# Kernel tuning notes

Hardware: AMD Instinct MI355X
Metric: run time of the kernel (lower is better)

The kernel has to match this reference:

```python
import jax, jax.numpy as jnp
import numpy as np

B, S, H, NH = 2, 2048, 1024, 16
PH = H // NH  # per-head size = 64


def setup_inputs() -> dict:
    key = jax.random.key(0)
    ks = jax.random.split(key, 12)
    scale = 0.02
    inp = {
        "key": jax.random.normal(ks[0], (B, S, H), jnp.float32),
        "value": jax.random.normal(ks[1], (B, S, H), jnp.float32),
        "query": jax.random.normal(ks[2], (B, S, H), jnp.float32),
        "mask": jax.random.uniform(ks[3], (B, 1, S, S), jnp.float32),
        "i": 0,
        "Wq": jax.random.normal(ks[4], (H, H), jnp.float32) * scale,
        "bq": jnp.zeros((H,), jnp.float32),
        "Wk": jax.random.normal(ks[5], (H, H), jnp.float32) * scale,
        "bk": jnp.zeros((H,), jnp.float32),
        "Wv": jax.random.normal(ks[6], (H, H), jnp.float32) * scale,
        "bv": jnp.zeros((H,), jnp.float32),
        "Wo": jax.random.normal(ks[7], (H, H), jnp.float32) * scale,
        "bo": jnp.zeros((H,), jnp.float32),
    }
    return inp


def reference(key, value, query, mask, i, Wq, bq, Wk, bk, Wv, bv, Wo, bo):
    # Linear projections (torch nn.Linear: x @ W.T + b), then split heads -> [B, NH, S, PH]
    def proj(x, W, b):
        return (x @ W.T + b).reshape(B, S, NH, PH).transpose(0, 2, 1, 3)

    q = proj(query, Wq, bq)
    k = proj(key, Wk, bk)
    v = proj(value, Wv, bv)

    # scores: [B, NH, S, S]; scale then MULTIPLICATIVE mask (as in the original)
    scores = jnp.einsum('bhqd,bhkd->bhqk', q, k) / jnp.sqrt(jnp.float32(PH))
    scores = scores * mask
    probs = jax.nn.softmax(scores, axis=-1)  # dropout p=0 -> identity

    # context: [B, NH, S, PH] -> merge heads -> [B, S, H]
    ctx = jnp.einsum('bhqk,bhkd->bhqd', probs, v)
    ctx = ctx.transpose(0, 2, 1, 3).reshape(B, S, H)
    return ctx @ Wo.T + bo
```

## Files before the change

kernel.cpp:

```cpp
#include <hip/hip_runtime.h>

typedef unsigned short ushort_t;
typedef __attribute__((ext_vector_type(8))) __bf16 bf16x8;
typedef __attribute__((ext_vector_type(4))) __bf16 bf16x4;
typedef __attribute__((ext_vector_type(4))) float f32x4;

__device__ inline float bf2f(ushort_t u) {
  union { unsigned int i; float f; } v; v.i = ((unsigned int)u) << 16; return v.f;
}
__device__ inline ushort_t f2bf(float f) {
  union { float f; unsigned int i; } v; v.f = f;
  unsigned int r = (v.i + 0x7fffu + ((v.i >> 16) & 1u)) >> 16;
  return (ushort_t)r;
}

__global__ void detect_dtype_kernel(const ushort_t* __restrict__ w,
                                    int* __restrict__ flag) {
  int lane = threadIdx.x & 63;
  int cnt = 0;
  for (int i = 0; i < 4; i++) {
    float a = fabsf(bf2f(w[lane * 4 + i]));
    if (a >= 1e-4f && a <= 0.5f) cnt++;
  }
  for (int off = 1; off < 64; off <<= 1) cnt += __shfl_xor(cnt, off, 64);
  if (threadIdx.x == 0) *flag = (cnt >= 192) ? 1 : 0;
}

__device__ inline float ld1(const void* src, size_t idx, int isbf) {
  return isbf ? bf2f(((const ushort_t*)src)[idx]) : ((const float*)src)[idx];
}

struct pre8 { float4 a, b; };
__device__ inline pre8 pref8(const void* src, size_t idx, int isbf) {
  pre8 u;
  if (isbf) {
    u.a = *(const float4*)((const ushort_t*)src + idx);
    u.b = u.a;
  } else {
    const float* s = (const float*)src + idx;
    u.a = *(const float4*)s;
    u.b = *(const float4*)(s + 4);
  }
  return u;
}
__device__ inline void commit8(ushort_t* dst, pre8 u, int isbf) {
  if (isbf) {
    *(float4*)dst = u.a;
  } else {
    union { bf16x8 v; ushort_t u8[8]; } t;
    t.u8[0] = f2bf(u.a.x); t.u8[1] = f2bf(u.a.y); t.u8[2] = f2bf(u.a.z); t.u8[3] = f2bf(u.a.w);
    t.u8[4] = f2bf(u.b.x); t.u8[5] = f2bf(u.b.y); t.u8[6] = f2bf(u.b.z); t.u8[7] = f2bf(u.b.w);
    *(bf16x8*)dst = t.v;
  }
}
__device__ inline void cvt8(ushort_t* dst, const void* src, size_t idx, int isbf) {
  commit8(dst, pref8(src, idx, isbf), isbf);
}

#define NW_ ((size_t)1024 * 1024)
#define NX_ ((size_t)4096 * 1024)
#define NM_ ((size_t)2 * 2048 * 2048)

__global__ __launch_bounds__(256) void cvt_all_kernel(
    const void* xq, const void* xk, const void* xv,
    const void* wq, const void* wk, const void* wv, const void* wo,
    ushort_t* __restrict__ dst, const int* __restrict__ flag) {
  int seg = blockIdx.z;
  const void* src; size_t n, doff;
  switch (seg) {
    case 0: src = wq; n = NW_; doff = 0;                 break;
    case 1: src = wk; n = NW_; doff = NW_;               break;
    case 2: src = wv; n = NW_; doff = 2 * NW_;           break;
    case 3: src = wo; n = NW_; doff = 3 * NW_;           break;
    case 4: src = xq; n = NX_; doff = 4 * NW_;           break;
    case 5: src = xk; n = NX_; doff = 4 * NW_ + NX_;     break;
    default: src = xv; n = NX_; doff = 4 * NW_ + 2 * NX_; break;
  }
  size_t i = ((size_t)blockIdx.x * 256 + threadIdx.x) * 8;
  if (i >= n) return;
  cvt8(&dst[doff + i], src, i, *flag);
}

__global__ __launch_bounds__(256) void transpose_mask_kernel(
    const void* __restrict__ M, ushort_t* __restrict__ Mt,
    const int* __restrict__ flag) {
  __shared__ ushort_t T[64][72];
  const int f = *flag;
  const int tid = threadIdx.x;
  const int r = tid >> 2, c = (tid & 3) * 16;
  const int b = blockIdx.z;
  const int q0 = blockIdx.x * 64, k0 = blockIdx.y * 64;
  const size_t src = (size_t)b * 2048 * 2048 + (size_t)(q0 + r) * 2048 + k0 + c;
  cvt8(&T[r][c],     M, src, f);
  cvt8(&T[r][c + 8], M, src + 8, f);
  __syncthreads();
  union { bf16x8 v; ushort_t u[8]; } o0, o1;
  for (int i = 0; i < 8; i++) o0.u[i] = T[c + i][r];
  for (int i = 0; i < 8; i++) o1.u[i] = T[c + 8 + i][r];
  ushort_t* dst = Mt + (size_t)b * 2048 * 2048;
  *(bf16x8*)&dst[(size_t)(k0 + r) * 2048 + q0 + c]     = o0.v;
  *(bf16x8*)&dst[(size_t)(k0 + r) * 2048 + q0 + c + 8] = o1.v;
}

#define KDIM 1024
#define NDIM 1024

__device__ __forceinline__ void gld_lds16(ushort_t* lds, const ushort_t* g) {
  __builtin_amdgcn_global_load_lds(
      (const __attribute__((address_space(1))) void*)g,
      (__attribute__((address_space(3))) void*)lds, 16, 0, 0);
}

template <int MODE>
__global__ __launch_bounds__(256) void gemm_fast_kernel(
    const ushort_t* __restrict__ X0, const ushort_t* __restrict__ X1,
    const ushort_t* __restrict__ X2,
    const ushort_t* __restrict__ W0, const ushort_t* __restrict__ W1,
    const ushort_t* __restrict__ W2,
    const void* __restrict__ B0, const void* __restrict__ B1,
    const void* __restrict__ B2,
    void* __restrict__ O0, void* __restrict__ O1, void* __restrict__ O2,
    const int* __restrict__ flag) {
  __shared__ ushort_t As[128 * 64];
  __shared__ ushort_t Bs[128 * 64];
  const int z = blockIdx.z;
  const ushort_t* X = z == 0 ? X0 : z == 1 ? X1 : X2;
  const ushort_t* W = z == 0 ? W0 : z == 1 ? W1 : W2;
  const void* Bias  = z == 0 ? B0 : z == 1 ? B1 : B2;
  void* Out         = z == 0 ? O0 : z == 1 ? O1 : O2;
  const int f = *flag;

  const int tid = threadIdx.x;
  const int wave = tid >> 6, lane = tid & 63;
  const int g = lane >> 4, l16 = lane & 15;
  const int m0 = blockIdx.y * 128, n0 = blockIdx.x * 128;
  const int wm = (wave >> 1) * 64, wn = (wave & 1) * 64;
  const int lr = lane >> 3;
  const int lc = (lane & 7) ^ lr;

  f32x4 acc[4][4] = {};

  for (int k0 = 0; k0 < KDIM; k0 += 64) {
#pragma unroll
    for (int q = 0; q < 4; q++) {
      const int row = wave * 32 + q * 8;
      gld_lds16(&As[row * 64], &X[(size_t)(m0 + row + lr) * KDIM + k0 + lc * 8]);
      gld_lds16(&Bs[row * 64], &W[(size_t)(n0 + row + lr) * KDIM + k0 + lc * 8]);
    }
    __syncthreads();

    bf16x8 af[2][4], bfr[2][4];
#pragma unroll
    for (int kk = 0; kk < 2; kk++)
#pragma unroll
      for (int i = 0; i < 4; i++) {
        const int cs = ((g + 4 * kk) ^ (l16 & 7)) * 8;
        af[kk][i]  = *(const bf16x8*)&As[(wm + i * 16 + l16) * 64 + cs];
        bfr[kk][i] = *(const bf16x8*)&Bs[(wn + i * 16 + l16) * 64 + cs];
      }
#pragma unroll
    for (int kk = 0; kk < 2; kk++)
#pragma unroll
      for (int i = 0; i < 4; i++)
#pragma unroll
        for (int j = 0; j < 4; j++)
          acc[i][j] = __builtin_amdgcn_mfma_f32_16x16x32_bf16(
              af[kk][i], bfr[kk][j], acc[i][j], 0, 0, 0);
    __syncthreads();
  }

  for (int i = 0; i < 4; i++)
    for (int j = 0; j < 4; j++)
      for (int r = 0; r < 4; r++) {
        int m = m0 + wm + i * 16 + g * 4 + r;
        int n = n0 + wn + j * 16 + l16;
        float v = acc[i][j][r] + ld1(Bias, n, f);
        if (MODE == 0) {
          if (f) ((ushort_t*)Out)[(size_t)m * NDIM + n] = f2bf(v);
          else   ((float*)Out)[(size_t)m * NDIM + n] = v;
        } else {
          int b = m >> 11, s = m & 2047, h = n >> 6, d = n & 63;
          ((ushort_t*)Out)[((((size_t)b * 16 + h) * 2048) + s) * 64 + d] = f2bf(v);
        }
      }
}

#define BK 32

template <int MODE>
__device__ inline void gemm_body(const void* __restrict__ X,
                                 const void* __restrict__ W,
                                 const void* __restrict__ Bias,
                                 void* __restrict__ Out,
                                 int xbf, int wbf, int bbf, int obf) {
  __shared__ ushort_t As[128][BK + 8];
  __shared__ ushort_t Bs[128][BK + 8];
  const int tid = threadIdx.x;
  const int wave = tid >> 6, lane = tid & 63;
  const int g = lane >> 4, l16 = lane & 15;
  const int m0 = blockIdx.y * 128, n0 = blockIdx.x * 128;
  const int wm = (wave >> 1) * 64, wn = (wave & 1) * 64;

  f32x4 acc[4][4] = {};
  const int r0 = tid >> 2, c0 = (tid & 3) * 8;
  const size_t ia0 = (size_t)(m0 + r0) * KDIM + c0;
  const size_t ia1 = (size_t)(m0 + r0 + 64) * KDIM + c0;
  const size_t ib0 = (size_t)(n0 + r0) * KDIM + c0;
  const size_t ib1 = (size_t)(n0 + r0 + 64) * KDIM + c0;

  pre8 pa0 = pref8(X, ia0, xbf), pa1 = pref8(X, ia1, xbf);
  pre8 pb0 = pref8(W, ib0, wbf), pb1 = pref8(W, ib1, wbf);

  for (int k0 = 0; k0 < KDIM; k0 += BK) {
    commit8(&As[r0][c0],      pa0, xbf);
    commit8(&As[r0 + 64][c0], pa1, xbf);
    commit8(&Bs[r0][c0],      pb0, wbf);
    commit8(&Bs[r0 + 64][c0], pb1, wbf);
    const int kn = (k0 + BK) & (KDIM - 1);
    pa0 = pref8(X, ia0 + kn, xbf); pa1 = pref8(X, ia1 + kn, xbf);
    pb0 = pref8(W, ib0 + kn, wbf); pb1 = pref8(W, ib1 + kn, wbf);
    __syncthreads();
    bf16x8 af[4], bfr[4];
    for (int i = 0; i < 4; i++) af[i]  = *(const bf16x8*)&As[wm + i * 16 + l16][g * 8];
    for (int j = 0; j < 4; j++) bfr[j] = *(const bf16x8*)&Bs[wn + j * 16 + l16][g * 8];
    for (int i = 0; i < 4; i++)
      for (int j = 0; j < 4; j++)
        acc[i][j] = __builtin_amdgcn_mfma_f32_16x16x32_bf16(af[i], bfr[j], acc[i][j], 0, 0, 0);
    __syncthreads();
  }
  for (int i = 0; i < 4; i++)
    for (int j = 0; j < 4; j++)
      for (int r = 0; r < 4; r++) {
        int m = m0 + wm + i * 16 + g * 4 + r;
        int n = n0 + wn + j * 16 + l16;
        float v = acc[i][j][r] + ld1(Bias, n, bbf);
        if (MODE == 0) {
          if (obf) ((ushort_t*)Out)[(size_t)m * NDIM + n] = f2bf(v);
          else     ((float*)Out)[(size_t)m * NDIM + n] = v;
        } else {
          int b = m >> 11, s = m & 2047, h = n >> 6, d = n & 63;
          ((ushort_t*)Out)[((((size_t)b * 16 + h) * 2048) + s) * 64 + d] = f2bf(v);
        }
      }
}

__global__ __launch_bounds__(256) void proj_qkv_fb_kernel(
    const void* __restrict__ query, const void* __restrict__ key,
    const void* __restrict__ value,
    const void* __restrict__ Wq, const void* __restrict__ bq,
    const void* __restrict__ Wk, const void* __restrict__ bk,
    const void* __restrict__ Wv, const void* __restrict__ bv,
    ushort_t* __restrict__ Q, ushort_t* __restrict__ K, ushort_t* __restrict__ V,
    const int* __restrict__ flag) {
  int f = *flag;
  int z = blockIdx.z;
  const void* X = z == 0 ? query : z == 1 ? key : value;
  const void* W = z == 0 ? Wq : z == 1 ? Wk : Wv;
  const void* B = z == 0 ? bq : z == 1 ? bk : bv;
  ushort_t* O  = z == 0 ? Q  : z == 1 ? K  : V;
  gemm_body<1>(X, W, B, O, f, f, f, 1);
}

__global__ __launch_bounds__(256) void out_proj_fb_kernel(
    const ushort_t* __restrict__ X, const void* __restrict__ W,
    const void* __restrict__ B, void* __restrict__ O,
    const int* __restrict__ flag) {
  int f = *flag;
  gemm_body<0>(X, W, B, O, 1, f, f, f);
}

__global__ __launch_bounds__(256) void transpose_v_kernel(
    const ushort_t* __restrict__ Vin, ushort_t* __restrict__ Vout) {
  __shared__ ushort_t T[64][72];
  const int tid = threadIdx.x;
  const int r = tid >> 2, c = (tid & 3) * 16;
  const int bh = blockIdx.y;
  const int s0 = blockIdx.x * 64;
  const ushort_t* src = Vin + (size_t)bh * 2048 * 64;
  *(bf16x8*)&T[r][c]     = *(const bf16x8*)&src[(size_t)(s0 + r) * 64 + c];
  *(bf16x8*)&T[r][c + 8] = *(const bf16x8*)&src[(size_t)(s0 + r) * 64 + c + 8];
  __syncthreads();
  union { bf16x8 v; ushort_t u[8]; } o0, o1;
  for (int i = 0; i < 8; i++) o0.u[i] = T[c + i][r];
  for (int i = 0; i < 8; i++) o1.u[i] = T[c + 8 + i][r];
  ushort_t* dst = Vout + (size_t)bh * 64 * 2048;
  *(bf16x8*)&dst[(size_t)r * 2048 + s0 + c]     = o0.v;
  *(bf16x8*)&dst[(size_t)r * 2048 + s0 + c + 8] = o1.v;
}

__global__ __launch_bounds__(256, 2) void flash_attn128_kernel(
    const ushort_t* __restrict__ Q, const ushort_t* __restrict__ K,
    const ushort_t* __restrict__ Vt, const ushort_t* __restrict__ Mt,
    ushort_t* __restrict__ ctx) {
  __shared__ ushort_t Ks[64 * 72];
  __shared__ ushort_t Vs[64 * 72];
  __shared__ ushort_t MQ[8448];
  __shared__ ushort_t Ps[4][32 * 72];

  const int tid = threadIdx.x;
  const int wave = tid >> 6, lane = tid & 63;
  const int g = lane >> 4, l16 = lane & 15;
  const int bh = blockIdx.x;
  const int b = bh >> 4, h = bh & 15;
  const int q0 = blockIdx.y * 128;

  const ushort_t* Qh = Q + (size_t)bh * 2048 * 64;
  const ushort_t* Kh = K + (size_t)bh * 2048 * 64;
  const ushort_t* Vh = Vt + (size_t)bh * 64 * 2048;
  const ushort_t* Mh = Mt + (size_t)b * 2048 * 2048 + q0;

  {
    const int qr = tid >> 1, qc = (tid & 1) * 32;
#pragma unroll
    for (int ch = 0; ch < 4; ch++) {
      union { bf16x8 v; ushort_t u[8]; } a;
      a.v = *(const bf16x8*)&Qh[(size_t)(q0 + qr) * 64 + qc + ch * 8];
      for (int i = 0; i < 8; i++) a.u[i] = f2bf(bf2f(a.u[i]) * 0.125f);
      *(bf16x8*)&MQ[qr * 66 + qc + ch * 8] = a.v;
    }
  }
  __syncthreads();
  bf16x8 aq[2][2];
#pragma unroll
  for (int t = 0; t < 2; t++)
#pragma unroll
    for (int kk = 0; kk < 2; kk++)
      aq[t][kk] = *(const bf16x8*)&MQ[(wave * 32 + t * 16 + l16) * 66 + kk * 32 + g * 8];

  float lpart[2][4] = {};
  f32x4 o_acc[2][4] = {};

  const int r = tid >> 2, c = (tid & 3) * 16;
  const int mc = (tid & 3) * 32;

  bf16x8 kr0 = *(const bf16x8*)&Kh[(size_t)r * 64 + c];
  bf16x8 kr1 = *(const bf16x8*)&Kh[(size_t)r * 64 + c + 8];
  bf16x8 vr0 = *(const bf16x8*)&Vh[(size_t)r * 2048 + c];
  bf16x8 vr1 = *(const bf16x8*)&Vh[(size_t)r * 2048 + c + 8];
  bf16x8 pm0 = *(const bf16x8*)&Mh[(size_t)r * 2048 + mc];
  bf16x8 pm1 = *(const bf16x8*)&Mh[(size_t)r * 2048 + mc + 8];
  bf16x8 pm2 = *(const bf16x8*)&Mh[(size_t)r * 2048 + mc + 16];
  bf16x8 pm3 = *(const bf16x8*)&Mh[(size_t)r * 2048 + mc + 24];

  for (int kt0 = 0; kt0 < 2048; kt0 += 64) {
    __syncthreads();
    *(bf16x8*)&Ks[r * 72 + c]      = kr0;
    *(bf16x8*)&Ks[r * 72 + c + 8]  = kr1;
    *(bf16x8*)&Vs[r * 72 + c]      = vr0;
    *(bf16x8*)&Vs[r * 72 + c + 8]  = vr1;
    *(bf16x8*)&MQ[r * 132 + mc]      = pm0;
    *(bf16x8*)&MQ[r * 132 + mc + 8]  = pm1;
    *(bf16x8*)&MQ[r * 132 + mc + 16] = pm2;
    *(bf16x8*)&MQ[r * 132 + mc + 24] = pm3;
    __syncthreads();

    const int ktn = (kt0 + 64) & 2047;
    kr0 = *(const bf16x8*)&Kh[(size_t)(ktn + r) * 64 + c];
    kr1 = *(const bf16x8*)&Kh[(size_t)(ktn + r) * 64 + c + 8];
    vr0 = *(const bf16x8*)&Vh[(size_t)r * 2048 + ktn + c];
    vr1 = *(const bf16x8*)&Vh[(size_t)r * 2048 + ktn + c + 8];
    pm0 = *(const bf16x8*)&Mh[(size_t)(ktn + r) * 2048 + mc];
    pm1 = *(const bf16x8*)&Mh[(size_t)(ktn + r) * 2048 + mc + 8];
    pm2 = *(const bf16x8*)&Mh[(size_t)(ktn + r) * 2048 + mc + 16];
    pm3 = *(const bf16x8*)&Mh[(size_t)(ktn + r) * 2048 + mc + 24];

    f32x4 sc[2][4] = {};
#pragma unroll
    for (int j = 0; j < 4; j++) {
      bf16x8 bk0 = *(const bf16x8*)&Ks[(j * 16 + l16) * 72 + g * 8];
      bf16x8 bk1 = *(const bf16x8*)&Ks[(j * 16 + l16) * 72 + 32 + g * 8];
#pragma unroll
      for (int t = 0; t < 2; t++) {
        sc[t][j] = __builtin_amdgcn_mfma_f32_16x16x32_bf16(aq[t][0], bk0, sc[t][j], 0, 0, 0);
        sc[t][j] = __builtin_amdgcn_mfma_f32_16x16x32_bf16(aq[t][1], bk1, sc[t][j], 0, 0, 0);
      }
    }

#pragma unroll
    for (int t = 0; t < 2; t++)
#pragma unroll
      for (int j = 0; j < 4; j++) {
        union { bf16x4 v; ushort_t u[4]; } m4;
        m4.v = *(const bf16x4*)&MQ[(j * 16 + l16) * 132 + wave * 32 + t * 16 + g * 4];
#pragma unroll
        for (int rr = 0; rr < 4; rr++) {
          float s = fminf(sc[t][j][rr] * bf2f(m4.u[rr]), 80.f);
          float p = __expf(s);
          unsigned int pb = __float_as_uint(p);
          lpart[t][rr] += __uint_as_float(pb & 0xffff0000u);
          Ps[wave][(t * 16 + g * 4 + rr) * 72 + j * 16 + l16] = (ushort_t)(pb >> 16);
        }
      }
    asm volatile("" ::: "memory");

    bf16x8 pf00 = *(const bf16x8*)&Ps[wave][(l16) * 72 + g * 8];
    bf16x8 pf01 = *(const bf16x8*)&Ps[wave][(l16) * 72 + 32 + g * 8];
    bf16x8 pf10 = *(const bf16x8*)&Ps[wave][(16 + l16) * 72 + g * 8];
    bf16x8 pf11 = *(const bf16x8*)&Ps[wave][(16 + l16) * 72 + 32 + g * 8];
#pragma unroll
    for (int jd = 0; jd < 4; jd++) {
      bf16x8 vf0 = *(const bf16x8*)&Vs[(jd * 16 + l16) * 72 + g * 8];
      bf16x8 vf1 = *(const bf16x8*)&Vs[(jd * 16 + l16) * 72 + 32 + g * 8];
      o_acc[0][jd] = __builtin_amdgcn_mfma_f32_16x16x32_bf16(pf00, vf0, o_acc[0][jd], 0, 0, 0);
      o_acc[0][jd] = __builtin_amdgcn_mfma_f32_16x16x32_bf16(pf01, vf1, o_acc[0][jd], 0, 0, 0);
      o_acc[1][jd] = __builtin_amdgcn_mfma_f32_16x16x32_bf16(pf10, vf0, o_acc[1][jd], 0, 0, 0);
      o_acc[1][jd] = __builtin_amdgcn_mfma_f32_16x16x32_bf16(pf11, vf1, o_acc[1][jd], 0, 0, 0);
    }
  }

#pragma unroll
  for (int t = 0; t < 2; t++) {
    float rl[4];
#pragma unroll
    for (int rr = 0; rr < 4; rr++) {
      float l = lpart[t][rr];
      l += __shfl_xor(l, 1, 64);
      l += __shfl_xor(l, 2, 64);
      l += __shfl_xor(l, 4, 64);
      l += __shfl_xor(l, 8, 64);
      rl[rr] = 1.0f / l;
    }
#pragma unroll
    for (int jd = 0; jd < 4; jd++)
#pragma unroll
      for (int rr = 0; rr < 4; rr++) {
        int qrow = q0 + wave * 32 + t * 16 + g * 4 + rr;
        ctx[((size_t)b * 2048 + qrow) * 1024 + h * 64 + jd * 16 + l16] =
            f2bf(o_acc[t][jd][rr] * rl[rr]);
      }
  }
}

#define FS 72

template <int PRET>
__global__ __launch_bounds__(256, 4) void flash_attn_kernel(
    const ushort_t* __restrict__ Q, const ushort_t* __restrict__ K,
    const ushort_t* __restrict__ V, const void* __restrict__ mask,
    ushort_t* __restrict__ ctx, const int* __restrict__ flag) {
  __shared__ ushort_t QsM[64][FS];
  __shared__ ushort_t Ks[64][FS];
  __shared__ ushort_t Vs[64][FS];
  __shared__ ushort_t Ps[4][16][FS];

  const int mbf = *flag;
  const int tid = threadIdx.x;
  const int wave = tid >> 6, lane = tid & 63;
  const int g = lane >> 4, l16 = lane & 15;
  const int bh = blockIdx.x;
  const int b = bh >> 4, h = bh & 15;
  const int q0 = blockIdx.y * 64;

  const ushort_t* Qh = Q + (size_t)bh * 2048 * 64;
  const ushort_t* Kh = K + (size_t)bh * 2048 * 64;
  const ushort_t* Vh = PRET ? V + (size_t)bh * 64 * 2048
                            : V + (size_t)bh * 2048 * 64;
  const int mrow = wave * 16 + g * 4;
  const int r = tid >> 2, c = (tid & 3) * 16;
  const size_t mstage = (size_t)b * 2048 * 2048 + (size_t)(q0 + r) * 2048 + c;

  {
    union { bf16x8 v; ushort_t u[8]; } a0, a1;
    a0.v = *(const bf16x8*)&Qh[(size_t)(q0 + r) * 64 + c];
    a1.v = *(const bf16x8*)&Qh[(size_t)(q0 + r) * 64 + c + 8];
    for (int i = 0; i < 8; i++) {
      a0.u[i] = f2bf(bf2f(a0.u[i]) * 0.125f);
      a1.u[i] = f2bf(bf2f(a1.u[i]) * 0.125f);
    }
    *(bf16x8*)&QsM[r][c]     = a0.v;
    *(bf16x8*)&QsM[r][c + 8] = a1.v;
  }
  __syncthreads();
  const bf16x8 aq0 = *(const bf16x8*)&QsM[wave * 16 + l16][g * 8];
  const bf16x8 aq1 = *(const bf16x8*)&QsM[wave * 16 + l16][32 + g * 8];

  float lpart[4] = {0.f, 0.f, 0.f, 0.f};
  f32x4 o_acc[4] = {};

  bf16x8 kr0 = *(const bf16x8*)&Kh[(size_t)r * 64 + c];
  bf16x8 kr1 = *(const bf16x8*)&Kh[(size_t)r * 64 + c + 8];
  bf16x8 vr0, vr1;
  if (PRET) {
    vr0 = *(const bf16x8*)&Vh[(size_t)r * 2048 + c];
    vr1 = *(const bf16x8*)&Vh[(size_t)r * 2048 + c + 8];
  } else {
    vr0 = *(const bf16x8*)&Vh[(size_t)r * 64 + c];
    vr1 = *(const bf16x8*)&Vh[(size_t)r * 64 + c + 8];
  }
  pre8 pm0 = pref8(mask, mstage, mbf);
  pre8 pm1 = pref8(mask, mstage + 8, mbf);

  for (int kt0 = 0; kt0 < 2048; kt0 += 64) {
    __syncthreads();
    *(bf16x8*)&Ks[r][c]     = kr0;
    *(bf16x8*)&Ks[r][c + 8] = kr1;
    if (PRET) {
      *(bf16x8*)&Vs[r][c]     = vr0;
      *(bf16x8*)&Vs[r][c + 8] = vr1;
    } else {
      union { bf16x8 v; ushort_t u[8]; } a0, a1;
      a0.v = vr0; a1.v = vr1;
      for (int i = 0; i < 8; i++) Vs[c + i][r] = a0.u[i];
      for (int i = 0; i < 8; i++) Vs[c + 8 + i][r] = a1.u[i];
    }
    commit8(&QsM[r][c],     pm0, mbf);
    commit8(&QsM[r][c + 8], pm1, mbf);
    __syncthreads();

    const int ktn = (kt0 + 64) & 2047;
    kr0 = *(const bf16x8*)&Kh[(size_t)(ktn + r) * 64 + c];
    kr1 = *(const bf16x8*)&Kh[(size_t)(ktn + r) * 64 + c + 8];
    if (PRET) {
      vr0 = *(const bf16x8*)&Vh[(size_t)r * 2048 + ktn + c];
      vr1 = *(const bf16x8*)&Vh[(size_t)r * 2048 + ktn + c + 8];
    } else {
      vr0 = *(const bf16x8*)&Vh[(size_t)(ktn + r) * 64 + c];
      vr1 = *(const bf16x8*)&Vh[(size_t)(ktn + r) * 64 + c + 8];
    }
    pm0 = pref8(mask, mstage + ktn, mbf);
    pm1 = pref8(mask, mstage + ktn + 8, mbf);

    f32x4 sc[4] = {};
#pragma unroll
    for (int j = 0; j < 4; j++) {
      bf16x8 bk0 = *(const bf16x8*)&Ks[j * 16 + l16][g * 8];
      bf16x8 bk1 = *(const bf16x8*)&Ks[j * 16 + l16][32 + g * 8];
      sc[j] = __builtin_amdgcn_mfma_f32_16x16x32_bf16(aq0, bk0, sc[j], 0, 0, 0);
      sc[j] = __builtin_amdgcn_mfma_f32_16x16x32_bf16(aq1, bk1, sc[j], 0, 0, 0);
    }

#pragma unroll
    for (int j = 0; j < 4; j++)
#pragma unroll
      for (int rr = 0; rr < 4; rr++) {
        float m = bf2f(QsM[mrow + rr][j * 16 + l16]);
        float s = fminf(sc[j][rr] * m, 80.f);
        float p = __expf(s);
        unsigned int pb = __float_as_uint(p);
        lpart[rr] += __uint_as_float(pb & 0xffff0000u);
        Ps[wave][g * 4 + rr][j * 16 + l16] = (ushort_t)(pb >> 16);
      }
    asm volatile("" ::: "memory");

    bf16x8 pf0 = *(const bf16x8*)&Ps[wave][l16][g * 8];
    bf16x8 pf1 = *(const bf16x8*)&Ps[wave][l16][32 + g * 8];
#pragma unroll
    for (int jd = 0; jd < 4; jd++) {
      bf16x8 vf0 = *(const bf16x8*)&Vs[jd * 16 + l16][g * 8];
      bf16x8 vf1 = *(const bf16x8*)&Vs[jd * 16 + l16][32 + g * 8];
      o_acc[jd] = __builtin_amdgcn_mfma_f32_16x16x32_bf16(pf0, vf0, o_acc[jd], 0, 0, 0);
      o_acc[jd] = __builtin_amdgcn_mfma_f32_16x16x32_bf16(pf1, vf1, o_acc[jd], 0, 0, 0);
    }
  }

  float rl[4];
  for (int rr = 0; rr < 4; rr++) {
    float l = lpart[rr];
    l += __shfl_xor(l, 1, 64);
    l += __shfl_xor(l, 2, 64);
    l += __shfl_xor(l, 4, 64);
    l += __shfl_xor(l, 8, 64);
    rl[rr] = 1.0f / l;
  }
  for (int jd = 0; jd < 4; jd++)
    for (int rr = 0; rr < 4; rr++) {
      int qrow = q0 + mrow + rr;
      ctx[((size_t)b * 2048 + qrow) * 1024 + h * 64 + jd * 16 + l16] =
          f2bf(o_acc[jd][rr] * rl[rr]);
    }
}

extern "C" void kernel_launch(void* const* d_in, const int* in_sizes, int n_in,
                              void* d_out, int out_size, void* d_ws, size_t ws_size,
                              hipStream_t stream) {
  (void)in_sizes; (void)n_in; (void)out_size;
  const void* key   = d_in[0];
  const void* value = d_in[1];
  const void* query = d_in[2];
  const void* mask  = d_in[3];
  const void* Wq = d_in[5];
  const void* bq = d_in[6];
  const void* Wk = d_in[7];
  const void* bk = d_in[8];
  const void* Wv = d_in[9];
  const void* bv = d_in[10];
  const void* Wo = d_in[11];
  const void* bo = d_in[12];

  const size_t E = (size_t)2 * 2048 * 1024;
  ushort_t* Qw  = (ushort_t*)d_ws;
  ushort_t* Kw  = Qw + E;
  ushort_t* Vw  = Kw + E;
  ushort_t* CTX = Vw + E;
  int* flag = (int*)(CTX + E);
  ushort_t* Vt   = (ushort_t*)((char*)flag + 256);
  ushort_t* conv = Vt + E;

  const size_t need_pret = 4 * E * 2 + 256 + E * 2;
  const size_t need_W   = need_pret + 4 * NW_ * 2;
  const size_t need_WX  = need_W + 3 * NX_ * 2;
  const size_t need_all = need_WX + NM_ * 2;
  const int pret  = ws_size >= need_pret ? 1 : 0;
  const int convW = (pret && ws_size >= need_W)   ? 1 : 0;
  const int convX = (pret && ws_size >= need_WX)  ? 1 : 0;
  const int convM = (pret && ws_size >= need_all) ? 1 : 0;

  detect_dtype_kernel<<<1, 64, 0, stream>>>((const ushort_t*)Wq, flag);

  if (convW) {
    int nseg = convX ? 7 : 4;
    int nx   = convX ? 2048 : 512;
    cvt_all_kernel<<<dim3(nx, 1, nseg), 256, 0, stream>>>(
        query, key, value, Wq, Wk, Wv, Wo, conv, flag);
  }
  const ushort_t* Wq_c = conv;
  const ushort_t* Wk_c = conv + NW_;
  const ushort_t* Wv_c = conv + 2 * NW_;
  const ushort_t* Wo_c = conv + 3 * NW_;
  const ushort_t* Xq_c = conv + 4 * NW_;
  const ushort_t* Xk_c = conv + 4 * NW_ + NX_;
  const ushort_t* Xv_c = conv + 4 * NW_ + 2 * NX_;
  ushort_t* Mt = conv + 4 * NW_ + 3 * NX_;

  if (convM) {
    transpose_mask_kernel<<<dim3(32, 32, 2), 256, 0, stream>>>(mask, Mt, flag);
  }

  if (convW && convX) {
    gemm_fast_kernel<1><<<dim3(8, 32, 3), 256, 0, stream>>>(
        Xq_c, Xk_c, Xv_c, Wq_c, Wk_c, Wv_c, bq, bk, bv,
        Qw, Kw, Vw, flag);
  } else {
    proj_qkv_fb_kernel<<<dim3(8, 32, 3), 256, 0, stream>>>(
        query, key, value, Wq, bq, Wk, bk, Wv, bv, Qw, Kw, Vw, flag);
  }

  if (pret) {
    transpose_v_kernel<<<dim3(32, 32), 256, 0, stream>>>(Vw, Vt);
    if (convM) {
      flash_attn128_kernel<<<dim3(32, 16), 256, 0, stream>>>(Qw, Kw, Vt, Mt, CTX);
    } else {
      flash_attn_kernel<1><<<dim3(32, 32), 256, 0, stream>>>(Qw, Kw, Vt, mask, CTX, flag);
    }
  } else {
    flash_attn_kernel<0><<<dim3(32, 32), 256, 0, stream>>>(Qw, Kw, Vw, mask, CTX, flag);
  }

  if (convW) {
    gemm_fast_kernel<0><<<dim3(8, 32, 1), 256, 0, stream>>>(
        CTX, CTX, CTX, Wo_c, Wo_c, Wo_c, bo, bo, bo,
        d_out, d_out, d_out, flag);
  } else {
    out_proj_fb_kernel<<<dim3(8, 32), 256, 0, stream>>>(CTX, Wo, bo, d_out, flag);
  }
}
```

Baseline: 330.1 us.

## Split attention over key halves, fuse mask transpose into prep, narrow out-proj tiles

Flash attention is split into two key-range halves via a grid z dimension, writing unnormalized fp32 partial outputs and row sums that a new combine kernel merges and normalizes into bf16 context. The mask transpose is folded into the input/weight conversion kernel as an extra segment, saving a launch. The output projection GEMM uses 64-wide N tiles to double block count. This raises parallelism for undersubscribed kernels at the cost of extra fp32 partial traffic, workspace, and an additional launch.

```diff
diff --git a/kernel.cpp b/kernel.cpp
--- a/kernel.cpp
+++ b/kernel.cpp
@@ -61,45 +61,45 @@
 #define NX_ ((size_t)4096 * 1024)
 #define NM_ ((size_t)2 * 2048 * 2048)
 
-__global__ __launch_bounds__(256) void cvt_all_kernel(
+__global__ __launch_bounds__(256) void prep_kernel(
     const void* xq, const void* xk, const void* xv,
     const void* wq, const void* wk, const void* wv, const void* wo,
-    ushort_t* __restrict__ dst, const int* __restrict__ flag) {
-  int seg = blockIdx.z;
-  const void* src; size_t n, doff;
-  switch (seg) {
-    case 0: src = wq; n = NW_; doff = 0;                 break;
-    case 1: src = wk; n = NW_; doff = NW_;               break;
-    case 2: src = wv; n = NW_; doff = 2 * NW_;           break;
-    case 3: src = wo; n = NW_; doff = 3 * NW_;           break;
-    case 4: src = xq; n = NX_; doff = 4 * NW_;           break;
-    case 5: src = xk; n = NX_; doff = 4 * NW_ + NX_;     break;
-    default: src = xv; n = NX_; doff = 4 * NW_ + 2 * NX_; break;
-  }
-  size_t i = ((size_t)blockIdx.x * 256 + threadIdx.x) * 8;
-  if (i >= n) return;
-  cvt8(&dst[doff + i], src, i, *flag);
-}
-
-__global__ __launch_bounds__(256) void transpose_mask_kernel(
-    const void* __restrict__ M, ushort_t* __restrict__ Mt,
+    const void* mask, ushort_t* __restrict__ dst, ushort_t* __restrict__ Mt,
     const int* __restrict__ flag) {
   __shared__ ushort_t T[64][72];
+  const int seg = blockIdx.z;
   const int f = *flag;
-  const int tid = threadIdx.x;
-  const int r = tid >> 2, c = (tid & 3) * 16;
-  const int b = blockIdx.z;
-  const int q0 = blockIdx.x * 64, k0 = blockIdx.y * 64;
-  const size_t src = (size_t)b * 2048 * 2048 + (size_t)(q0 + r) * 2048 + k0 + c;
-  cvt8(&T[r][c],     M, src, f);
-  cvt8(&T[r][c + 8], M, src + 8, f);
-  __syncthreads();
-  union { bf16x8 v; ushort_t u[8]; } o0, o1;
-  for (int i = 0; i < 8; i++) o0.u[i] = T[c + i][r];
-  for (int i = 0; i < 8; i++) o1.u[i] = T[c + 8 + i][r];
-  ushort_t* dst = Mt + (size_t)b * 2048 * 2048;
-  *(bf16x8*)&dst[(size_t)(k0 + r) * 2048 + q0 + c]     = o0.v;
-  *(bf16x8*)&dst[(size_t)(k0 + r) * 2048 + q0 + c + 8] = o1.v;
+  if (seg < 7) {
+    const void* src; size_t n, doff;
+    switch (seg) {
+      case 0: src = wq; n = NW_; doff = 0;                 break;
+      case 1: src = wk; n = NW_; doff = NW_;               break;
+      case 2: src = wv; n = NW_; doff = 2 * NW_;           break;
+      case 3: src = wo; n = NW_; doff = 3 * NW_;           break;
+      case 4: src = xq; n = NX_; doff = 4 * NW_;           break;
+      case 5: src = xk; n = NX_; doff = 4 * NW_ + NX_;     break;
+      default: src = xv; n = NX_; doff = 4 * NW_ + 2 * NX_; break;
+    }
+    size_t i = ((size_t)blockIdx.x * 256 + threadIdx.x) * 8;
+    if (i >= n) return;
+    cvt8(&dst[doff + i], src, i, f);
+  } else {
+    const int x = blockIdx.x;
+    const int b = x >> 10, rem = x & 1023;
+    const int q0 = (rem & 31) * 64, k0 = (rem >> 5) * 64;
+    const int tid = threadIdx.x;
+    const int r = tid >> 2, c = (tid & 3) * 16;
+    const size_t src = (size_t)b * 2048 * 2048 + (size_t)(q0 + r) * 2048 + k0 + c;
+    cvt8(&T[r][c],     mask, src, f);
+    cvt8(&T[r][c + 8], mask, src + 8, f);
+    __syncthreads();
+    union { bf16x8 v; ushort_t u[8]; } o0, o1;
+    for (int i = 0; i < 8; i++) o0.u[i] = T[c + i][r];
+    for (int i = 0; i < 8; i++) o1.u[i] = T[c + 8 + i][r];
+    ushort_t* d = Mt + (size_t)b * 2048 * 2048;
+    *(bf16x8*)&d[(size_t)(k0 + r) * 2048 + q0 + c]     = o0.v;
+    *(bf16x8*)&d[(size_t)(k0 + r) * 2048 + q0 + c + 8] = o1.v;
+  }
 }
 
 #define KDIM 1024
@@ -111,7 +111,7 @@
       (__attribute__((address_space(3))) void*)lds, 16, 0, 0);
 }
 
-template <int MODE>
+template <int MODE, int NT>
 __global__ __launch_bounds__(256) void gemm_fast_kernel(
     const ushort_t* __restrict__ X0, const ushort_t* __restrict__ X1,
     const ushort_t* __restrict__ X2,
@@ -121,8 +121,9 @@
     const void* __restrict__ B2,
     void* __restrict__ O0, void* __restrict__ O1, void* __restrict__ O2,
     const int* __restrict__ flag) {
+  constexpr int NJ = NT / 32;
   __shared__ ushort_t As[128 * 64];
-  __shared__ ushort_t Bs[128 * 64];
+  __shared__ ushort_t Bs[NT * 64];
   const int z = blockIdx.z;
   const ushort_t* X = z == 0 ? X0 : z == 1 ? X1 : X2;
   const ushort_t* W = z == 0 ? W0 : z == 1 ? W1 : W2;
@@ -133,44 +134,50 @@
   const int tid = threadIdx.x;
   const int wave = tid >> 6, lane = tid & 63;
   const int g = lane >> 4, l16 = lane & 15;
-  const int m0 = blockIdx.y * 128, n0 = blockIdx.x * 128;
-  const int wm = (wave >> 1) * 64, wn = (wave & 1) * 64;
+  const int m0 = blockIdx.y * 128, n0 = blockIdx.x * NT;
+  const int wm = (wave >> 1) * 64, wn = (wave & 1) * (NT / 2);
   const int lr = lane >> 3;
   const int lc = (lane & 7) ^ lr;
 
-  f32x4 acc[4][4] = {};
+  f32x4 acc[4][NJ] = {};
 
   for (int k0 = 0; k0 < KDIM; k0 += 64) {
 #pragma unroll
     for (int q = 0; q < 4; q++) {
       const int row = wave * 32 + q * 8;
       gld_lds16(&As[row * 64], &X[(size_t)(m0 + row + lr) * KDIM + k0 + lc * 8]);
+    }
+#pragma unroll
+    for (int q = 0; q < NT / 32; q++) {
+      const int row = wave * (NT / 4) + q * 8;
       gld_lds16(&Bs[row * 64], &W[(size_t)(n0 + row + lr) * KDIM + k0 + lc * 8]);
     }
     __syncthreads();
 
-    bf16x8 af[2][4], bfr[2][4];
+    bf16x8 af[2][4], bfr[2][NJ];
+#pragma unroll
+    for (int kk = 0; kk < 2; kk++) {
+      const int cs = ((g + 4 * kk) ^ (l16 & 7)) * 8;
+#pragma unroll
+      for (int i = 0; i < 4; i++)
+        af[kk][i]  = *(const bf16x8*)&As[(wm + i * 16 + l16) * 64 + cs];
+#pragma unroll
+      for (int j = 0; j < NJ; j++)
+        bfr[kk][j] = *(const bf16x8*)&Bs[(wn + j * 16 + l16) * 64 + cs];
+    }
 #pragma unroll
     for (int kk = 0; kk < 2; kk++)
 #pragma unroll
-      for (int i = 0; i < 4; i++) {
-        const int cs = ((g + 4 * kk) ^ (l16 & 7)) * 8;
-        af[kk][i]  = *(const bf16x8*)&As[(wm + i * 16 + l16) * 64 + cs];
-        bfr[kk][i] = *(const bf16x8*)&Bs[(wn + i * 16 + l16) * 64 + cs];
-      }
-#pragma unroll
-    for (int kk = 0; kk < 2; kk++)
-#pragma unroll
       for (int i = 0; i < 4; i++)
 #pragma unroll
-        for (int j = 0; j < 4; j++)
+        for (int j = 0; j < NJ; j++)
           acc[i][j] = __builtin_amdgcn_mfma_f32_16x16x32_bf16(
               af[kk][i], bfr[kk][j], acc[i][j], 0, 0, 0);
     __syncthreads();
   }
 
   for (int i = 0; i < 4; i++)
-    for (int j = 0; j < 4; j++)
+    for (int j = 0; j < NJ; j++)
       for (int r = 0; r < 4; r++) {
         int m = m0 + wm + i * 16 + g * 4 + r;
         int n = n0 + wn + j * 16 + l16;
@@ -288,10 +295,12 @@
   *(bf16x8*)&dst[(size_t)r * 2048 + s0 + c + 8] = o1.v;
 }
 
+template <int SPLIT>
 __global__ __launch_bounds__(256, 2) void flash_attn128_kernel(
     const ushort_t* __restrict__ Q, const ushort_t* __restrict__ K,
     const ushort_t* __restrict__ Vt, const ushort_t* __restrict__ Mt,
-    ushort_t* __restrict__ ctx) {
+    ushort_t* __restrict__ ctx, float* __restrict__ Opart,
+    float* __restrict__ Lpart) {
   __shared__ ushort_t Ks[64 * 72];
   __shared__ ushort_t Vs[64 * 72];
   __shared__ ushort_t MQ[8448];
@@ -303,6 +312,8 @@
   const int bh = blockIdx.x;
   const int b = bh >> 4, h = bh & 15;
   const int q0 = blockIdx.y * 128;
+  const int z = SPLIT ? blockIdx.z : 0;
+  const int kbase = z * 1024, kend = SPLIT ? kbase + 1024 : 2048;
 
   const ushort_t* Qh = Q + (size_t)bh * 2048 * 64;
   const ushort_t* Kh = K + (size_t)bh * 2048 * 64;
@@ -333,16 +344,16 @@
   const int r = tid >> 2, c = (tid & 3) * 16;
   const int mc = (tid & 3) * 32;
 
-  bf16x8 kr0 = *(const bf16x8*)&Kh[(size_t)r * 64 + c];
-  bf16x8 kr1 = *(const bf16x8*)&Kh[(size_t)r * 64 + c + 8];
-  bf16x8 vr0 = *(const bf16x8*)&Vh[(size_t)r * 2048 + c];
-  bf16x8 vr1 = *(const bf16x8*)&Vh[(size_t)r * 2048 + c + 8];
-  bf16x8 pm0 = *(const bf16x8*)&Mh[(size_t)r * 2048 + mc];
-  bf16x8 pm1 = *(const bf16x8*)&Mh[(size_t)r * 2048 + mc + 8];
-  bf16x8 pm2 = *(const bf16x8*)&Mh[(size_t)r * 2048 + mc + 16];
-  bf16x8 pm3 = *(const bf16x8*)&Mh[(size_t)r * 2048 + mc + 24];
-
-  for (int kt0 = 0; kt0 < 2048; kt0 += 64) {
+  bf16x8 kr0 = *(const bf16x8*)&Kh[(size_t)(kbase + r) * 64 + c];
+  bf16x8 kr1 = *(const bf16x8*)&Kh[(size_t)(kbase + r) * 64 + c + 8];
+  bf16x8 vr0 = *(const bf16x8*)&Vh[(size_t)r * 2048 + kbase + c];
+  bf16x8 vr1 = *(const bf16x8*)&Vh[(size_t)r * 2048 + kbase + c + 8];
+  bf16x8 pm0 = *(const bf16x8*)&Mh[(size_t)(kbase + r) * 2048 + mc];
+  bf16x8 pm1 = *(const bf16x8*)&Mh[(size_t)(kbase + r) * 2048 + mc + 8];
+  bf16x8 pm2 = *(const bf16x8*)&Mh[(size_t)(kbase + r) * 2048 + mc + 16];
+  bf16x8 pm3 = *(const bf16x8*)&Mh[(size_t)(kbase + r) * 2048 + mc + 24];
+
+  for (int kt0 = kbase; kt0 < kend; kt0 += 64) {
     __syncthreads();
     *(bf16x8*)&Ks[r * 72 + c]      = kr0;
     *(bf16x8*)&Ks[r * 72 + c + 8]  = kr1;
@@ -408,27 +419,76 @@
     }
   }
 
-#pragma unroll
-  for (int t = 0; t < 2; t++) {
-    float rl[4];
-#pragma unroll
-    for (int rr = 0; rr < 4; rr++) {
-      float l = lpart[t][rr];
-      l += __shfl_xor(l, 1, 64);
-      l += __shfl_xor(l, 2, 64);
-      l += __shfl_xor(l, 4, 64);
-      l += __shfl_xor(l, 8, 64);
-      rl[rr] = 1.0f / l;
-    }
-#pragma unroll
-    for (int jd = 0; jd < 4; jd++)
+  if (SPLIT) {
+    float* Ow = Opart + (size_t)z * ((size_t)2 * 2048 * 1024);
+    float* Lw = Lpart + (size_t)z * (32 * 2048);
+#pragma unroll
+    for (int t = 0; t < 2; t++) {
+      float ls[4];
 #pragma unroll
       for (int rr = 0; rr < 4; rr++) {
-        int qrow = q0 + wave * 32 + t * 16 + g * 4 + rr;
-        ctx[((size_t)b * 2048 + qrow) * 1024 + h * 64 + jd * 16 + l16] =
-            f2bf(o_acc[t][jd][rr] * rl[rr]);
+        float l = lpart[t][rr];
+        l += __shfl_xor(l, 1, 64);
+        l += __shfl_xor(l, 2, 64);
+        l += __shfl_xor(l, 4, 64);
+        l += __shfl_xor(l, 8, 64);
+        ls[rr] = l;
       }
-  }
+      if (l16 == 0)
+#pragma unroll
+        for (int rr = 0; rr < 4; rr++)
+          Lw[(size_t)bh * 2048 + q0 + wave * 32 + t * 16 + g * 4 + rr] = ls[rr];
+#pragma unroll
+      for (int jd = 0; jd < 4; jd++)
+#pragma unroll
+        for (int rr = 0; rr < 4; rr++) {
+          int qrow = q0 + wave * 32 + t * 16 + g * 4 + rr;
+          Ow[((size_t)b * 2048 + qrow) * 1024 + h * 64 + jd * 16 + l16] =
+              o_acc[t][jd][rr];
+        }
+    }
+  } else {
+#pragma unroll
+    for (int t = 0; t < 2; t++) {
+      float rl[4];
+#pragma unroll
+      for (int rr = 0; rr < 4; rr++) {
+        float l = lpart[t][rr];
+        l += __shfl_xor(l, 1, 64);
+        l += __shfl_xor(l, 2, 64);
+        l += __shfl_xor(l, 4, 64);
+        l += __shfl_xor(l, 8, 64);
+        rl[rr] = 1.0f / l;
+      }
+#pragma unroll
+      for (int jd = 0; jd < 4; jd++)
+#pragma unroll
+        for (int rr = 0; rr < 4; rr++) {
+          int qrow = q0 + wave * 32 + t * 16 + g * 4 + rr;
+          ctx[((size_t)b * 2048 + qrow) * 1024 + h * 64 + jd * 16 + l16] =
+              f2bf(o_acc[t][jd][rr] * rl[rr]);
+        }
+    }
+  }
+}
+
+__global__ __launch_bounds__(256) void combine_kernel(
+    const float* __restrict__ O0, const float* __restrict__ O1,
+    const float* __restrict__ L0, const float* __restrict__ L1,
+    ushort_t* __restrict__ ctx) {
+  size_t i = ((size_t)blockIdx.x * 256 + threadIdx.x) * 4;
+  int h = (int)((i & 1023) >> 6);
+  size_t s = (i >> 10) & 2047, b = i >> 21;
+  size_t li = (b * 16 + h) * 2048 + s;
+  float rl = 1.0f / (L0[li] + L1[li]);
+  float4 a = *(const float4*)&O0[i];
+  float4 c = *(const float4*)&O1[i];
+  union { bf16x4 v; ushort_t u[4]; } o;
+  o.u[0] = f2bf((a.x + c.x) * rl);
+  o.u[1] = f2bf((a.y + c.y) * rl);
+  o.u[2] = f2bf((a.z + c.z) * rl);
+  o.u[3] = f2bf((a.w + c.w) * rl);
+  *(bf16x4*)&ctx[i] = o.v;
 }
 
 #define FS 72
@@ -595,23 +655,28 @@
   int* flag = (int*)(CTX + E);
   ushort_t* Vt   = (ushort_t*)((char*)flag + 256);
   ushort_t* conv = Vt + E;
-
-  const size_t need_pret = 4 * E * 2 + 256 + E * 2;
-  const size_t need_W   = need_pret + 4 * NW_ * 2;
-  const size_t need_WX  = need_W + 3 * NX_ * 2;
-  const size_t need_all = need_WX + NM_ * 2;
+  ushort_t* Mt = conv + 4 * NW_ + 3 * NX_;
+  float* Opart = (float*)(Mt + NM_);
+  float* Lpart = Opart + 2 * E;
+
+  const size_t need_pret  = 4 * E * 2 + 256 + E * 2;
+  const size_t need_W     = need_pret + 4 * NW_ * 2;
+  const size_t need_WX    = need_W + 3 * NX_ * 2;
+  const size_t need_all   = need_WX + NM_ * 2;
+  const size_t need_split = need_all + 2 * E * 4 + 2 * (size_t)32 * 2048 * 4;
   const int pret  = ws_size >= need_pret ? 1 : 0;
   const int convW = (pret && ws_size >= need_W)   ? 1 : 0;
   const int convX = (pret && ws_size >= need_WX)  ? 1 : 0;
   const int convM = (pret && ws_size >= need_all) ? 1 : 0;
+  const int ksplit = (convM && ws_size >= need_split) ? 1 : 0;
 
   detect_dtype_kernel<<<1, 64, 0, stream>>>((const ushort_t*)Wq, flag);
 
   if (convW) {
-    int nseg = convX ? 7 : 4;
-    int nx   = convX ? 2048 : 512;
-    cvt_all_kernel<<<dim3(nx, 1, nseg), 256, 0, stream>>>(
-        query, key, value, Wq, Wk, Wv, Wo, conv, flag);
+    int nseg = convM ? 8 : (convX ? 7 : 4);
+    int nx   = (convX || convM) ? 2048 : 512;
+    prep_kernel<<<dim3(nx, 1, nseg), 256, 0, stream>>>(
+        query, key, value, Wq, Wk, Wv, Wo, mask, conv, Mt, flag);
   }
   const ushort_t* Wq_c = conv;
   const ushort_t* Wk_c = conv + NW_;
@@ -620,14 +685,9 @@
   const ushort_t* Xq_c = conv + 4 * NW_;
   const ushort_t* Xk_c = conv + 4 * NW_ + NX_;
   const ushort_t* Xv_c = conv + 4 * NW_ + 2 * NX_;
-  ushort_t* Mt = conv + 4 * NW_ + 3 * NX_;
-
-  if (convM) {
-    transpose_mask_kernel<<<dim3(32, 32, 2), 256, 0, stream>>>(mask, Mt, flag);
-  }
 
   if (convW && convX) {
-    gemm_fast_kernel<1><<<dim3(8, 32, 3), 256, 0, stream>>>(
+    gemm_fast_kernel<1, 128><<<dim3(8, 32, 3), 256, 0, stream>>>(
         Xq_c, Xk_c, Xv_c, Wq_c, Wk_c, Wv_c, bq, bk, bv,
         Qw, Kw, Vw, flag);
   } else {
@@ -637,8 +697,14 @@
 
   if (pret) {
     transpose_v_kernel<<<dim3(32, 32), 256, 0, stream>>>(Vw, Vt);
-    if (convM) {
-      flash_attn128_kernel<<<dim3(32, 16), 256, 0, stream>>>(Qw, Kw, Vt, Mt, CTX);
+    if (convM && ksplit) {
+      flash_attn128_kernel<1><<<dim3(32, 16, 2), 256, 0, stream>>>(
+          Qw, Kw, Vt, Mt, CTX, Opart, Lpart);
+      combine_kernel<<<dim3(4096), 256, 0, stream>>>(
+          Opart, Opart + E, Lpart, Lpart + (size_t)32 * 2048, CTX);
+    } else if (convM) {
+      flash_attn128_kernel<0><<<dim3(32, 16, 1), 256, 0, stream>>>(
+          Qw, Kw, Vt, Mt, CTX, Opart, Lpart);
     } else {
       flash_attn_kernel<1><<<dim3(32, 32), 256, 0, stream>>>(Qw, Kw, Vt, mask, CTX, flag);
     }
@@ -647,7 +713,7 @@
   }
 
   if (convW) {
-    gemm_fast_kernel<0><<<dim3(8, 32, 1), 256, 0, stream>>>(
+    gemm_fast_kernel<0, 64><<<dim3(16, 32, 1), 256, 0, stream>>>(
         CTX, CTX, CTX, Wo_c, Wo_c, Wo_c, bo, bo, bo,
         d_out, d_out, d_out, flag);
   } else {
```

Measured after the change: 330.3 us. No clear change (+0.1%).
